# Kernel tuning notes

Hardware: AMD Instinct MI355X
Metric: run time of the kernel (lower is better)

Reference implementation:

```python
import jax, jax.numpy as jnp
import numpy as np

ALPHA = 0.1
ONE_MINUS_ALPHA = 1.0 - ALPHA
EPSILON = 1e-3
B, T, F = 16, 4096, 512


def setup_inputs() -> dict:
    key = jax.random.key(0)
    x = jax.random.normal(key, (B, T, F), dtype=jnp.float32)
    # init_state: stack of running-mean zeros and running-mean-square ones
    state = jnp.stack([jnp.zeros((B, F), jnp.float32), jnp.ones((B, F), jnp.float32)], axis=0)  # [2,B,F]
    return {"x": x, "state": state}


def reference(x, state):
    # p = alpha * [x, x^2] stacked: [2, B, T, F]
    p = ALPHA * jnp.stack([x, x * x], axis=0)
    p_t = jnp.moveaxis(p, 2, 0)  # [T, 2, B, F] — scan over time

    def step(s, pt):
        s = pt + ONE_MINUS_ALPHA * s
        return s, s

    final_state, states = jax.lax.scan(step, state, p_t)  # states: [T, 2, B, F]
    state_vector = jnp.moveaxis(states, 0, 2)  # [2, B, T, F]
    mean_vector = state_vector[0]
    var_vector = state_vector[1] - mean_vector * mean_vector
    x_norm = (x - mean_vector) / jnp.sqrt(var_vector + EPSILON)
    return (x_norm, final_state)
```

## Files before the change

kernel.cpp:

```cpp
#include <hip/hip_runtime.h>


namespace {
constexpr int Bc = 16, Tc = 4096, Fc = 512;
constexpr int CL = 256;
constexpr int KH = 128;
constexpr int NCHUNK = Tc / CL;
constexpr float ALPHA = 0.1f;
constexpr float OMA = 0.9f;
constexpr float EPS = 1e-3f;
}

__global__ __launch_bounds__(256) void tn_kernel(const float* __restrict__ x,
                                                 const float* __restrict__ state,
                                                 float* __restrict__ out) {
    const int bid = blockIdx.x;
    const int fh = bid & 1;
    const int chunk = (bid >> 1) & (NCHUNK - 1);
    const int b = bid >> 5;
    const int f = fh * 256 + threadIdx.x;
    const int t0 = chunk * CL;

    const size_t base = ((size_t)b * Tc + t0) * Fc + f;
    const float* xp = x + base;

    float s_m, s_v;
    if (chunk == 0) {
        s_m = state[b * Fc + f];
        s_v = state[Bc * Fc + b * Fc + f];
    } else {
        s_m = 0.f;
        s_v = 0.f;
        const float* wp = xp - (size_t)KH * Fc;
#pragma unroll 8
        for (int i = 0; i < KH; ++i) {
            float xv = wp[(size_t)i * Fc];
            float px = ALPHA * xv;
            s_m = fmaf(OMA, s_m, px);
            s_v = fmaf(OMA, s_v, px * xv);
        }
    }

    float* op = out + base;
#pragma unroll 8
    for (int i = 0; i < CL; ++i) {
        float xv = xp[(size_t)i * Fc];
        float px = ALPHA * xv;
        s_m = fmaf(OMA, s_m, px);
        s_v = fmaf(OMA, s_v, px * xv);
        float var = fmaf(-s_m, s_m, s_v);
        op[(size_t)i * Fc] = (xv - s_m) * rsqrtf(var + EPS);
    }

    if (chunk == NCHUNK - 1) {
        const size_t so = (size_t)Bc * Tc * Fc;
        out[so + (size_t)b * Fc + f] = s_m;
        out[so + (size_t)Bc * Fc + (size_t)b * Fc + f] = s_v;
    }
}

extern "C" void kernel_launch(void* const* d_in, const int* in_sizes, int n_in,
                              void* d_out, int out_size, void* d_ws, size_t ws_size,
                              hipStream_t stream) {
    const float* x = (const float*)d_in[0];
    const float* st = (const float*)d_in[1];
    float* out = (float*)d_out;

    dim3 grid(Bc * NCHUNK * 2);
    dim3 block(256);
    tn_kernel<<<grid, block, 0, stream>>>(x, st, out);
}
```

Before: 56.62 us.

## Vectorize scan to float4 per thread, halve chunk length, use nontemporal stores

```diff
diff --git a/kernel.cpp b/kernel.cpp
--- a/kernel.cpp
+++ b/kernel.cpp
@@ -3,70 +3,73 @@
 
 namespace {
 constexpr int Bc = 16, Tc = 4096, Fc = 512;
-constexpr int CL = 256;
+constexpr int CL = 128;
 constexpr int KH = 128;
 constexpr int NCHUNK = Tc / CL;
+constexpr int F4 = Fc / 4;
 constexpr float ALPHA = 0.1f;
 constexpr float OMA = 0.9f;
 constexpr float EPS = 1e-3f;
+typedef float v4 __attribute__((ext_vector_type(4)));
 }
 
-__global__ __launch_bounds__(256) void tn_kernel(const float* __restrict__ x,
-                                                 const float* __restrict__ state,
-                                                 float* __restrict__ out) {
-    const int bid = blockIdx.x;
-    const int fh = bid & 1;
-    const int chunk = (bid >> 1) & (NCHUNK - 1);
-    const int b = bid >> 5;
-    const int f = fh * 256 + threadIdx.x;
+__global__ __launch_bounds__(128) void tn_kernel(const v4* __restrict__ x4,
+                                                 const v4* __restrict__ st4,
+                                                 v4* __restrict__ out4) {
+    const int chunk = blockIdx.x & (NCHUNK - 1);
+    const int b = blockIdx.x >> 5;
+    const int f4 = threadIdx.x;
     const int t0 = chunk * CL;
 
-    const size_t base = ((size_t)b * Tc + t0) * Fc + f;
-    const float* xp = x + base;
+    const size_t base = ((size_t)b * Tc + t0) * F4 + f4;
+    const v4* xp = x4 + base;
 
-    float s_m, s_v;
+    v4 s_m, s_v;
     if (chunk == 0) {
-        s_m = state[b * Fc + f];
-        s_v = state[Bc * Fc + b * Fc + f];
+        s_m = st4[(size_t)b * F4 + f4];
+        s_v = st4[(size_t)(Bc + b) * F4 + f4];
     } else {
-        s_m = 0.f;
-        s_v = 0.f;
-        const float* wp = xp - (size_t)KH * Fc;
+        s_m = (v4)0.f;
+        s_v = (v4)0.f;
+        const v4* wp = xp - (size_t)KH * F4;
 #pragma unroll 8
         for (int i = 0; i < KH; ++i) {
-            float xv = wp[(size_t)i * Fc];
-            float px = ALPHA * xv;
-            s_m = fmaf(OMA, s_m, px);
-            s_v = fmaf(OMA, s_v, px * xv);
+            v4 xv = wp[(size_t)i * F4];
+            v4 px = ALPHA * xv;
+            s_m = OMA * s_m + px;
+            s_v = OMA * s_v + px * xv;
         }
     }
 
-    float* op = out + base;
+    v4* op = out4 + base;
 #pragma unroll 8
     for (int i = 0; i < CL; ++i) {
-        float xv = xp[(size_t)i * Fc];
-        float px = ALPHA * xv;
-        s_m = fmaf(OMA, s_m, px);
-        s_v = fmaf(OMA, s_v, px * xv);
-        float var = fmaf(-s_m, s_m, s_v);
-        op[(size_t)i * Fc] = (xv - s_m) * rsqrtf(var + EPS);
+        v4 xv = xp[(size_t)i * F4];
+        v4 px = ALPHA * xv;
+        s_m = OMA * s_m + px;
+        s_v = OMA * s_v + px * xv;
+        v4 var = s_v - s_m * s_m + (v4)EPS;
+        v4 r;
+#pragma unroll
+        for (int c = 0; c < 4; ++c) r[c] = (xv[c] - s_m[c]) * rsqrtf(var[c]);
+        __builtin_nontemporal_store(r, &op[(size_t)i * F4]);
     }
 
     if (chunk == NCHUNK - 1) {
-        const size_t so = (size_t)Bc * Tc * Fc;
-        out[so + (size_t)b * Fc + f] = s_m;
-        out[so + (size_t)Bc * Fc + (size_t)b * Fc + f] = s_v;
+        const size_t so = (size_t)Bc * Tc * F4;
+        out4[so + (size_t)b * F4 + f4] = s_m;
+        out4[so + (size_t)(Bc + b) * F4 + f4] = s_v;
     }
 }
 
 extern "C" void kernel_launch(void* const* d_in, const int* in_sizes, int n_in,
                               void* d_out, int out_size, void* d_ws, size_t ws_size,
                               hipStream_t stream) {
-    const float* x = (const float*)d_in[0];
-    const float* st = (const float*)d_in[1];
-    float* out = (float*)d_out;
+    const v4* x = (const v4*)d_in[0];
+    const v4* st = (const v4*)d_in[1];
+    v4* out = (v4*)d_out;
 
-    dim3 grid(Bc * NCHUNK * 2);
-    dim3 block(256);
+    dim3 grid(Bc * NCHUNK);
+    dim3 block(128);
     tn_kernel<<<grid, block, 0, stream>>>(x, st, out);
 }
```

Result: slower. 64.89 us (+14.6%).
